# Kernel tuning notes

Hardware: AMD Instinct MI355X
Metric: run time of the kernel (lower is better)

The kernel has to match this reference:

```python
import jax, jax.numpy as jnp
import numpy as np

N, L = 4, 512
DN = 128   # node_feat_dim
DP = 64    # pair_feat_dim
H = 8      # num_heads
HD = 32    # hidden_dim per head
EPS = 1e-5


def _layer_norm(x, g, b):
    m = jnp.mean(x, axis=-1, keepdims=True)
    v = jnp.var(x, axis=-1, keepdims=True)
    return (x - m) / jnp.sqrt(v + EPS) * g + b


def setup_inputs() -> dict:
    key = jax.random.key(0)
    ks = jax.random.split(key, 12)
    w = lambda k, shape: (jax.random.normal(k, shape, jnp.float32)
                          / np.float32(np.sqrt(shape[0])))
    return {
        "x": jax.random.normal(ks[0], (N, L, DN), jnp.float32),
        "z": jax.random.normal(ks[1], (N, L, L, DP), jnp.float32),
        "Wq": w(ks[2], (DN, H * HD)),
        "Wk": w(ks[3], (DN, H * HD)),
        "Wv": w(ks[4], (DN, H * HD)),
        "Wp": w(ks[5], (DP, H)),
        "Wt1": w(ks[6], (H * HD + H * DP, DN)),
        "bt1": jnp.zeros((DN,), jnp.float32),
        "g1": jnp.ones((DN,), jnp.float32),
        "b1": jnp.zeros((DN,), jnp.float32),
        "W2a": w(ks[7], (DN, DN)),
        "b2a": jnp.zeros((DN,), jnp.float32),
        "W2b": w(ks[8], (DN, DN)),
        "b2b": jnp.zeros((DN,), jnp.float32),
        "g2": jnp.ones((DN,), jnp.float32),
        "b2": jnp.zeros((DN,), jnp.float32),
    }


def reference(x, z, Wq, Wk, Wv, Wp, Wt1, bt1, g1, b1,
              W2a, b2a, W2b, b2b, g2, b2):
    # projections -> (N, L, H, HD)
    q = (x @ Wq).reshape(N, L, H, HD)
    k = (x @ Wk).reshape(N, L, H, HD)
    v = (x @ Wv).reshape(N, L, H, HD)
    # pairwise node logits: (N, Li, Lj, H)
    logits_node = jnp.einsum('nihd,njhd->nijh', q, k) / np.float32(np.sqrt(HD))
    logits_pair = z @ Wp                                    # (N, Li, Lj, H)
    logits = (logits_node + logits_pair) * np.float32(np.sqrt(0.5))
    alpha = jax.nn.softmax(logits, axis=2)                  # softmax over j
    # aggregation
    feat_node = jnp.einsum('nijh,njhd->nihd', alpha, v).reshape(N, L, H * HD)
    feat_pair = jnp.einsum('nijh,nijp->nihp', alpha, z).reshape(N, L, H * DP)
    agg = jnp.concatenate([feat_node, feat_pair], axis=-1)  # (N, L, H*HD + H*DP)
    feats = _layer_norm(x + agg @ Wt1 + bt1, g1, b1)
    out = jax.nn.relu(feats @ W2a + b2a) @ W2b + b2b
    return _layer_norm(feats + out, g2, b2)
```

## Files before the change

### kernel.cpp

```cpp
#include <hip/hip_runtime.h>
#include <math.h>

#define NB 4
#define L 512
#define DN 128
#define DP 64
#define H 8
#define HD 32
#define NH (H*HD)
#define AGG (NH + H*DP)
#define JC 32
#define NCH (L/JC)

__device__ float g_qT[(size_t)NB*H*L*HD];
__device__ float g_kT[(size_t)NB*H*L*HD];
__device__ float g_v[NB*L*NH];
__device__ float g_agg[NB*L*AGG];
__device__ float g_nl[(size_t)NB*H*L*L];

__global__ __launch_bounds__(256) void k_qkv(const float* __restrict__ x,
    const float* __restrict__ Wq, const float* __restrict__ Wk,
    const float* __restrict__ Wv)
{
    __shared__ float xs[4*DN];
    int t = threadIdx.x;
    int rowbase = blockIdx.x * 4;
    #pragma unroll
    for (int it = 0; it < 2; ++it) {
        int flat = it*256 + t;
        xs[flat] = x[(size_t)rowbase*DN + flat];
    }
    __syncthreads();
    float aq[4], ak[4], av[4];
    #pragma unroll
    for (int r = 0; r < 4; ++r) { aq[r]=0.f; ak[r]=0.f; av[r]=0.f; }
    for (int d = 0; d < DN; ++d) {
        float wq = Wq[d*NH + t];
        float wk = Wk[d*NH + t];
        float wv = Wv[d*NH + t];
        #pragma unroll
        for (int r = 0; r < 4; ++r) {
            float xv = xs[r*DN + d];
            aq[r] = fmaf(xv, wq, aq[r]);
            ak[r] = fmaf(xv, wk, ak[r]);
            av[r] = fmaf(xv, wv, av[r]);
        }
    }
    int n2 = rowbase >> 9;
    int i0 = rowbase & 511;
    int h = t >> 5, d = t & 31;
    #pragma unroll
    for (int r = 0; r < 4; ++r) {
        size_t base = ((size_t)(n2*H + h)*L + i0 + r)*HD + d;
        g_qT[base] = aq[r] * 0.125f;
        g_kT[base] = ak[r];
        g_v[(size_t)(rowbase+r)*NH + t] = av[r];
    }
}

__global__ __launch_bounds__(256) void k_qk()
{
    __shared__ __align__(16) float qs[16*36];
    int t = threadIdx.x;
    int bid = blockIdx.x;
    int n = bid >> 8;
    int h = (bid >> 5) & 7;
    int i0 = (bid & 31) << 4;
    const float* qTb = g_qT + (size_t)((n*H + h)*L + i0)*HD;
    if (t < 128) {
        int row = t >> 3, c4 = (t & 7) << 2;
        float4 qv = *(const float4*)(qTb + row*HD + c4);
        *(float4*)&qs[row*36 + c4] = qv;
    }
    __syncthreads();
    const float* kTb = g_kT + (size_t)(n*H + h)*L*HD;
    for (int jc = 0; jc < L; jc += 256) {
        int j = jc + t;
        float4 kr[8];
        const float4* kb = (const float4*)(kTb + (size_t)j*HD);
        #pragma unroll
        for (int c4 = 0; c4 < 8; ++c4) kr[c4] = kb[c4];
        float* outb = g_nl + (size_t)((n*H + h)*L + i0)*L + j;
        #pragma unroll 4
        for (int i = 0; i < 16; ++i) {
            float a0 = 0.f, a1 = 0.f;
            #pragma unroll
            for (int c4 = 0; c4 < 8; c4 += 2) {
                float4 q0 = *(const float4*)&qs[i*36 + c4*4];
                float4 q1 = *(const float4*)&qs[i*36 + c4*4 + 4];
                a0 = fmaf(q0.x, kr[c4].x,   fmaf(q0.y, kr[c4].y,   a0));
                a0 = fmaf(q0.z, kr[c4].z,   fmaf(q0.w, kr[c4].w,   a0));
                a1 = fmaf(q1.x, kr[c4+1].x, fmaf(q1.y, kr[c4+1].y, a1));
                a1 = fmaf(q1.z, kr[c4+1].z, fmaf(q1.w, kr[c4+1].w, a1));
            }
            outb[(size_t)i*L] = a0 + a1;
        }
    }
}

#define ATTN_STEP(c, cur, NC, NN)                                              \
  {                                                                            \
    __syncthreads();                                                           \
    if ((c)+1 < NCH) {                                                         \
      _Pragma("unroll")                                                        \
      for (int it2 = 0; it2 < 2; ++it2) {                                      \
        int f4 = it2*256 + t, jj = f4 >> 4, p4 = (f4 & 15) << 2;               \
        float* d = &zc[(cur)^1][jj*65 + p4];                                   \
        d[0]=zR[it2].x; d[1]=zR[it2].y; d[2]=zR[it2].z; d[3]=zR[it2].w;        \
      }                                                                        \
    }                                                                          \
    if ((c)+2 < NCH) {                                                         \
      const float4* s2 = (const float4*)(zrow + (size_t)((c)+2)*JC*DP);        \
      zR[0]=s2[t]; zR[1]=s2[256+t];                                            \
    }                                                                          \
    if ((c)+1 < NCH) { NN = nlh[((c)+1)*JC + l32]; }                           \
    float va = NC, va1 = 0.f;                                                  \
    {                                                                          \
      const float* zr = &zc[cur][l32*65];                                      \
      _Pragma("unroll 16")                                                     \
      for (int pp = 0; pp < DP; pp += 2) {                                     \
        va  = fmaf(zr[pp],   wp[pp*H     + myh], va);                          \
        va1 = fmaf(zr[pp+1], wp[(pp+1)*H + myh], va1);                         \
      }                                                                        \
    }                                                                          \
    va += va1;                                                                 \
    float mx = va;                                                             \
    _Pragma("unroll")                                                          \
    for (int o = 16; o > 0; o >>= 1)                                           \
      mx = fmaxf(mx, __shfl_xor(mx, o));                                       \
    float mn = fmaxf(mh, mx);                                                  \
    float r  = __expf(mh - mn);                                                \
    float e  = __expf(va - mn);                                                \
    lcw[wv][hiHalf][l32] = e;                                                  \
    float se = e;                                                              \
    _Pragma("unroll")                                                          \
    for (int o = 16; o > 0; o >>= 1)                                           \
      se += __shfl_xor(se, o);                                                 \
    sh = sh*r + se; mh = mn;                                                   \
    float ra = __shfl(r, 0), rb = __shfl(r, 32);                               \
    accN *= r; accP0 *= ra; accP1 *= rb;                                       \
    const float* vbase = g_v + (size_t)(n*L + (c)*JC)*NH + hoff;               \
    const float* zcc = zc[cur];                                                \
    _Pragma("unroll 8")                                                        \
    for (int j = 0; j < JC; ++j) {                                             \
      float la = lcw[wv][0][j];                                                \
      float lb = lcw[wv][1][j];                                                \
      float vv = vbase[(size_t)j*NH];                                          \
      float zv = zcc[j*65 + lane];                                             \
      accN  = fmaf(hiHalf ? lb : la, vv, accN);                                \
      accP0 = fmaf(la, zv, accP0);                                             \
      accP1 = fmaf(lb, zv, accP1);                                             \
    }                                                                          \
  }

__global__ __launch_bounds__(256) void k_attn(const float* __restrict__ z,
    const float* __restrict__ Wp)
{
    __shared__ float zc[2][JC*65];
    __shared__ float lcw[4][2][JC];
    __shared__ float wp[DP*H];

    int t = threadIdx.x;
    int lane = t & 63;
    int wv = t >> 6;
    int row = blockIdx.x;
    int n = row >> 9;
    int i = row & 511;
    const float* zrow = z + (size_t)row * (L*DP);

    wp[t]       = Wp[t]       * 0.70710678118654752f;
    wp[t + 256] = Wp[t + 256] * 0.70710678118654752f;

    int hiHalf = lane >> 5;
    int l32 = lane & 31;
    int myh = wv + 4*hiHalf;
    const float* nlh = g_nl + ((size_t)((n*H + myh)*L + i))*L;

    int hoff = wv*32 + lane + (hiHalf ? 96 : 0);

    float accN = 0.f, accP0 = 0.f, accP1 = 0.f;
    float mh = -1e30f, sh = 0.f;

    float4 zR[2];
    float nlc, nln;

    {
        float4 zP[2];
        const float4* sp0 = (const float4*)zrow;
        zP[0] = sp0[t]; zP[1] = sp0[256 + t];
        nlc = nlh[l32];
        #pragma unroll
        for (int it = 0; it < 2; ++it) {
            int f4 = it*256 + t, jj = f4 >> 4, p4 = (f4 & 15) << 2;
            float* d = &zc[0][jj*65 + p4];
            d[0]=zP[it].x; d[1]=zP[it].y; d[2]=zP[it].z; d[3]=zP[it].w;
        }
        const float4* sp1 = (const float4*)(zrow + (size_t)JC*DP);
        zR[0] = sp1[t]; zR[1] = sp1[256 + t];
    }
    ATTN_STEP(0 ,0,nlc,nln)
    ATTN_STEP(1 ,1,nln,nlc)
    ATTN_STEP(2 ,0,nlc,nln)
    ATTN_STEP(3 ,1,nln,nlc)
    ATTN_STEP(4 ,0,nlc,nln)
    ATTN_STEP(5 ,1,nln,nlc)
    ATTN_STEP(6 ,0,nlc,nln)
    ATTN_STEP(7 ,1,nln,nlc)
    ATTN_STEP(8 ,0,nlc,nln)
    ATTN_STEP(9 ,1,nln,nlc)
    ATTN_STEP(10,0,nlc,nln)
    ATTN_STEP(11,1,nln,nlc)
    ATTN_STEP(12,0,nlc,nln)
    ATTN_STEP(13,1,nln,nlc)
    ATTN_STEP(14,0,nlc,nln)
    ATTN_STEP(15,1,nln,nlc)

    float s0 = __shfl(sh, 0), s1 = __shfl(sh, 32);
    float* arow = g_agg + (size_t)row * AGG;
    arow[hoff]                  = accN  * (1.f / sh);
    arow[NH + wv*DP + lane]     = accP0 * (1.f / s0);
    arow[NH + (wv+4)*DP + lane] = accP1 * (1.f / s1);
}

__global__ __launch_bounds__(256) void k_mlp(const float* __restrict__ x,
    const float* __restrict__ Wt1, const float* __restrict__ bt1,
    const float* __restrict__ g1, const float* __restrict__ b1,
    const float* __restrict__ W2a, const float* __restrict__ b2a,
    const float* __restrict__ W2b, const float* __restrict__ b2b,
    const float* __restrict__ g2, const float* __restrict__ b2,
    float* __restrict__ out)
{
    __shared__ float aggL[4*AGG];
    __shared__ float featsL[4*132];
    __shared__ float h1L[4*132];
    int t = threadIdx.x;
    int tc = t & 127;
    int tr = t >> 7;
    int lane = t & 63, wv = t >> 6;
    int rowbase = blockIdx.x * 4;

    #pragma unroll
    for (int it = 0; it < 12; ++it) {
        int flat = it*256 + t;
        aggL[flat] = g_agg[(size_t)rowbase*AGG + flat];
    }
    __syncthreads();
    float acc[2] = {0.f,0.f};
    for (int kk = 0; kk < AGG; ++kk) {
        float w = Wt1[kk*DN + tc];
        #pragma unroll
        for (int r = 0; r < 2; ++r)
            acc[r] = fmaf(aggL[(tr*2+r)*AGG + kk], w, acc[r]);
    }
    float bt = bt1[tc];
    #pragma unroll
    for (int r = 0; r < 2; ++r) {
        int row = tr*2 + r;
        featsL[row*132 + tc] = acc[r] + bt + x[(size_t)(rowbase+row)*DN + tc];
    }
    __syncthreads();
    {
        int row = wv;
        float v0 = featsL[row*132 + lane];
        float v1 = featsL[row*132 + 64 + lane];
        float s = v0 + v1, s2 = v0*v0 + v1*v1;
        #pragma unroll
        for (int o = 32; o > 0; o >>= 1) {
            s  += __shfl_xor(s,  o);
            s2 += __shfl_xor(s2, o);
        }
        float mean = s * (1.f/128.f);
        float var  = s2 * (1.f/128.f) - mean*mean;
        float rstd = rsqrtf(var + 1e-5f);
        featsL[row*132 + lane]      = (v0 - mean)*rstd*g1[lane]      + b1[lane];
        featsL[row*132 + 64 + lane] = (v1 - mean)*rstd*g1[64+lane]   + b1[64+lane];
    }
    __syncthreads();
    float acc2[2] = {0.f,0.f};
    for (int kk = 0; kk < DN; ++kk) {
        float w = W2a[kk*DN + tc];
        #pragma unroll
        for (int r = 0; r < 2; ++r)
            acc2[r] = fmaf(featsL[(tr*2+r)*132 + kk], w, acc2[r]);
    }
    float ba = b2a[tc];
    #pragma unroll
    for (int r = 0; r < 2; ++r)
        h1L[(tr*2+r)*132 + tc] = fmaxf(acc2[r] + ba, 0.f);
    __syncthreads();
    float acc3[2] = {0.f,0.f};
    for (int kk = 0; kk < DN; ++kk) {
        float w = W2b[kk*DN + tc];
        #pragma unroll
        for (int r = 0; r < 2; ++r)
            acc3[r] = fmaf(h1L[(tr*2+r)*132 + kk], w, acc3[r]);
    }
    float bb = b2b[tc];
    #pragma unroll
    for (int r = 0; r < 2; ++r) {
        int row = tr*2 + r;
        featsL[row*132 + tc] = featsL[row*132 + tc] + acc3[r] + bb;
    }
    __syncthreads();
    {
        int row = wv;
        float v0 = featsL[row*132 + lane];
        float v1 = featsL[row*132 + 64 + lane];
        float s = v0 + v1, s2 = v0*v0 + v1*v1;
        #pragma unroll
        for (int o = 32; o > 0; o >>= 1) {
            s  += __shfl_xor(s,  o);
            s2 += __shfl_xor(s2, o);
        }
        float mean = s * (1.f/128.f);
        float var  = s2 * (1.f/128.f) - mean*mean;
        float rstd = rsqrtf(var + 1e-5f);
        out[(size_t)(rowbase+row)*DN + lane]      = (v0 - mean)*rstd*g2[lane]    + b2[lane];
        out[(size_t)(rowbase+row)*DN + 64 + lane] = (v1 - mean)*rstd*g2[64+lane] + b2[64+lane];
    }
}

extern "C" void kernel_launch(void* const* d_in, const int* in_sizes, int n_in,
                              void* d_out, int out_size, void* d_ws, size_t ws_size,
                              hipStream_t stream) {
    const float* x   = (const float*)d_in[0];
    const float* z   = (const float*)d_in[1];
    const float* Wq  = (const float*)d_in[2];
    const float* Wk  = (const float*)d_in[3];
    const float* Wv  = (const float*)d_in[4];
    const float* Wp  = (const float*)d_in[5];
    const float* Wt1 = (const float*)d_in[6];
    const float* bt1 = (const float*)d_in[7];
    const float* g1  = (const float*)d_in[8];
    const float* b1  = (const float*)d_in[9];
    const float* W2a = (const float*)d_in[10];
    const float* b2a = (const float*)d_in[11];
    const float* W2b = (const float*)d_in[12];
    const float* b2b = (const float*)d_in[13];
    const float* g2  = (const float*)d_in[14];
    const float* b2  = (const float*)d_in[15];
    float* out = (float*)d_out;

    k_qkv<<<NB*L/4, 256, 0, stream>>>(x, Wq, Wk, Wv);
    k_qk<<<NB*H*(L/16), 256, 0, stream>>>();
    k_attn<<<NB*L, 256, 0, stream>>>(z, Wp);
    k_mlp<<<NB*L/4, 256, 0, stream>>>(x, Wt1, bt1, g1, b1,
                                      W2a, b2a, W2b, b2b, g2, b2, out);
}
```

Baseline: 205.1 us.

## Split pair-logit and softmax into separate kernel before attention aggregation

```diff
diff --git a/kernel.cpp b/kernel.cpp
--- a/kernel.cpp
+++ b/kernel.cpp
@@ -98,7 +98,67 @@
     }
 }
 
-#define ATTN_STEP(c, cur, NC, NN)                                              \
+__global__ __launch_bounds__(256) void k_pl(const float* __restrict__ z,
+    const float* __restrict__ Wp)
+{
+    __shared__ float wp[DP*H];
+    __shared__ float flt[H][L];
+    int t = threadIdx.x;
+    int lane = t & 63;
+    int wv = t >> 6;
+    int j0 = t & 63;
+    int n = blockIdx.x >> 9;
+    int i = blockIdx.x & 511;
+
+    wp[t]       = Wp[t]       * 0.70710678118654752f;
+    wp[t + 256] = Wp[t + 256] * 0.70710678118654752f;
+    __syncthreads();
+
+    const float* zbase = z + ((size_t)(n*L + i))*L*DP;
+    const float* nlA = g_nl + ((size_t)((n*H + wv    )*L + i))*L;
+    const float* nlB = g_nl + ((size_t)((n*H + wv + 4)*L + i))*L;
+
+    for (int jc = 0; jc < 8; ++jc) {
+        int j = jc*64 + j0;
+        const float* zr = zbase + (size_t)j*DP;
+        float va = nlA[j], vb = nlB[j];
+        float va1 = 0.f, vb1 = 0.f;
+        #pragma unroll 16
+        for (int p = 0; p < DP; p += 2) {
+            float z0 = zr[p], z1 = zr[p+1];
+            va  = fmaf(z0, wp[p*H     + wv],     va);
+            va1 = fmaf(z1, wp[(p+1)*H + wv],     va1);
+            vb  = fmaf(z0, wp[p*H     + wv + 4], vb);
+            vb1 = fmaf(z1, wp[(p+1)*H + wv + 4], vb1);
+        }
+        flt[wv][j]     = va + va1;
+        flt[wv + 4][j] = vb + vb1;
+    }
+    __syncthreads();
+    #pragma unroll
+    for (int hh = 0; hh < 2; ++hh) {
+        int head = wv + 4*hh;
+        float v[8];
+        #pragma unroll
+        for (int k = 0; k < 8; ++k) v[k] = flt[head][lane + k*64];
+        float m = v[0];
+        #pragma unroll
+        for (int k = 1; k < 8; ++k) m = fmaxf(m, v[k]);
+        #pragma unroll
+        for (int o = 32; o > 0; o >>= 1) m = fmaxf(m, __shfl_xor(m, o));
+        float s = 0.f;
+        #pragma unroll
+        for (int k = 0; k < 8; ++k) { v[k] = __expf(v[k] - m); s += v[k]; }
+        #pragma unroll
+        for (int o = 32; o > 0; o >>= 1) s += __shfl_xor(s, o);
+        float inv = 1.f / s;
+        float* outp = g_nl + ((size_t)((n*H + head)*L + i))*L;
+        #pragma unroll
+        for (int k = 0; k < 8; ++k) outp[lane + k*64] = v[k] * inv;
+    }
+}
+
+#define ATTN_STEP(c, cur)                                                      \
   {                                                                            \
     __syncthreads();                                                           \
     if ((c)+1 < NCH) {                                                         \
@@ -113,38 +173,12 @@
       const float4* s2 = (const float4*)(zrow + (size_t)((c)+2)*JC*DP);        \
       zR[0]=s2[t]; zR[1]=s2[256+t];                                            \
     }                                                                          \
-    if ((c)+1 < NCH) { NN = nlh[((c)+1)*JC + l32]; }                           \
-    float va = NC, va1 = 0.f;                                                  \
-    {                                                                          \
-      const float* zr = &zc[cur][l32*65];                                      \
-      _Pragma("unroll 16")                                                     \
-      for (int pp = 0; pp < DP; pp += 2) {                                     \
-        va  = fmaf(zr[pp],   wp[pp*H     + myh], va);                          \
-        va1 = fmaf(zr[pp+1], wp[(pp+1)*H + myh], va1);                         \
-      }                                                                        \
-    }                                                                          \
-    va += va1;                                                                 \
-    float mx = va;                                                             \
-    _Pragma("unroll")                                                          \
-    for (int o = 16; o > 0; o >>= 1)                                           \
-      mx = fmaxf(mx, __shfl_xor(mx, o));                                       \
-    float mn = fmaxf(mh, mx);                                                  \
-    float r  = __expf(mh - mn);                                                \
-    float e  = __expf(va - mn);                                                \
-    lcw[wv][hiHalf][l32] = e;                                                  \
-    float se = e;                                                              \
-    _Pragma("unroll")                                                          \
-    for (int o = 16; o > 0; o >>= 1)                                           \
-      se += __shfl_xor(se, o);                                                 \
-    sh = sh*r + se; mh = mn;                                                   \
-    float ra = __shfl(r, 0), rb = __shfl(r, 32);                               \
-    accN *= r; accP0 *= ra; accP1 *= rb;                                       \
     const float* vbase = g_v + (size_t)(n*L + (c)*JC)*NH + hoff;               \
     const float* zcc = zc[cur];                                                \
     _Pragma("unroll 8")                                                        \
     for (int j = 0; j < JC; ++j) {                                             \
-      float la = lcw[wv][0][j];                                                \
-      float lb = lcw[wv][1][j];                                                \
+      float la = al0[(c)*JC + j];                                              \
+      float lb = al4[(c)*JC + j];                                              \
       float vv = vbase[(size_t)j*NH];                                          \
       float zv = zcc[j*65 + lane];                                             \
       accN  = fmaf(hiHalf ? lb : la, vv, accN);                                \
@@ -153,12 +187,9 @@
     }                                                                          \
   }
 
-__global__ __launch_bounds__(256) void k_attn(const float* __restrict__ z,
-    const float* __restrict__ Wp)
+__global__ __launch_bounds__(256) void k_attn(const float* __restrict__ z)
 {
     __shared__ float zc[2][JC*65];
-    __shared__ float lcw[4][2][JC];
-    __shared__ float wp[DP*H];
 
     int t = threadIdx.x;
     int lane = t & 63;
@@ -168,27 +199,19 @@
     int i = row & 511;
     const float* zrow = z + (size_t)row * (L*DP);
 
-    wp[t]       = Wp[t]       * 0.70710678118654752f;
-    wp[t + 256] = Wp[t + 256] * 0.70710678118654752f;
+    const float* al0 = g_nl + ((size_t)((n*H + wv    )*L + i))*L;
+    const float* al4 = g_nl + ((size_t)((n*H + wv + 4)*L + i))*L;
 
     int hiHalf = lane >> 5;
-    int l32 = lane & 31;
-    int myh = wv + 4*hiHalf;
-    const float* nlh = g_nl + ((size_t)((n*H + myh)*L + i))*L;
-
     int hoff = wv*32 + lane + (hiHalf ? 96 : 0);
 
     float accN = 0.f, accP0 = 0.f, accP1 = 0.f;
-    float mh = -1e30f, sh = 0.f;
-
     float4 zR[2];
-    float nlc, nln;
 
     {
         float4 zP[2];
         const float4* sp0 = (const float4*)zrow;
         zP[0] = sp0[t]; zP[1] = sp0[256 + t];
-        nlc = nlh[l32];
         #pragma unroll
         for (int it = 0; it < 2; ++it) {
             int f4 = it*256 + t, jj = f4 >> 4, p4 = (f4 & 15) << 2;
@@ -198,28 +221,27 @@
         const float4* sp1 = (const float4*)(zrow + (size_t)JC*DP);
         zR[0] = sp1[t]; zR[1] = sp1[256 + t];
     }
-    ATTN_STEP(0 ,0,nlc,nln)
-    ATTN_STEP(1 ,1,nln,nlc)
-    ATTN_STEP(2 ,0,nlc,nln)
-    ATTN_STEP(3 ,1,nln,nlc)
-    ATTN_STEP(4 ,0,nlc,nln)
-    ATTN_STEP(5 ,1,nln,nlc)
-    ATTN_STEP(6 ,0,nlc,nln)
-    ATTN_STEP(7 ,1,nln,nlc)
-    ATTN_STEP(8 ,0,nlc,nln)
-    ATTN_STEP(9 ,1,nln,nlc)
-    ATTN_STEP(10,0,nlc,nln)
-    ATTN_STEP(11,1,nln,nlc)
-    ATTN_STEP(12,0,nlc,nln)
-    ATTN_STEP(13,1,nln,nlc)
-    ATTN_STEP(14,0,nlc,nln)
-    ATTN_STEP(15,1,nln,nlc)
-
-    float s0 = __shfl(sh, 0), s1 = __shfl(sh, 32);
+    ATTN_STEP(0 ,0)
+    ATTN_STEP(1 ,1)
+    ATTN_STEP(2 ,0)
+    ATTN_STEP(3 ,1)
+    ATTN_STEP(4 ,0)
+    ATTN_STEP(5 ,1)
+    ATTN_STEP(6 ,0)
+    ATTN_STEP(7 ,1)
+    ATTN_STEP(8 ,0)
+    ATTN_STEP(9 ,1)
+    ATTN_STEP(10,0)
+    ATTN_STEP(11,1)
+    ATTN_STEP(12,0)
+    ATTN_STEP(13,1)
+    ATTN_STEP(14,0)
+    ATTN_STEP(15,1)
+
     float* arow = g_agg + (size_t)row * AGG;
-    arow[hoff]                  = accN  * (1.f / sh);
-    arow[NH + wv*DP + lane]     = accP0 * (1.f / s0);
-    arow[NH + (wv+4)*DP + lane] = accP1 * (1.f / s1);
+    arow[hoff]                  = accN;
+    arow[NH + wv*DP + lane]     = accP0;
+    arow[NH + (wv+4)*DP + lane] = accP1;
 }
 
 __global__ __launch_bounds__(256) void k_mlp(const float* __restrict__ x,
@@ -343,7 +365,8 @@
 
     k_qkv<<<NB*L/4, 256, 0, stream>>>(x, Wq, Wk, Wv);
     k_qk<<<NB*H*(L/16), 256, 0, stream>>>();
-    k_attn<<<NB*L, 256, 0, stream>>>(z, Wp);
+    k_pl<<<NB*L, 256, 0, stream>>>(z, Wp);
+    k_attn<<<NB*L, 256, 0, stream>>>(z);
     k_mlp<<<NB*L/4, 256, 0, stream>>>(x, Wt1, bt1, g1, b1,
                                       W2a, b2a, W2b, b2b, g2, b2, out);
 }
```

Result: slower. 357.4 us (+74.2%).
